# Performance work log

Measured on AMD Instinct MI355X. Metric: run time of the kernel, lower is better.

## Reference

```python
import jax, jax.numpy as jnp
import numpy as np

NUM_HEADS = 16


def setup_inputs() -> dict:
    key = jax.random.key(0)
    k1, k2, k3 = jax.random.split(key, 3)
    B, S, C = 1, 4096, 1024
    x = jax.random.normal(k1, (B, S, C), dtype=jnp.float32)
    # additive causal mask: 0 on/below diagonal, -1e9 above
    causal = jnp.triu(jnp.full((S, S), -1e9, dtype=jnp.float32), k=1)
    attention_mask = causal[None, None, :, :]
    W_attn = jax.random.normal(k2, (C, 3 * C), dtype=jnp.float32) * (C ** -0.5)
    b_attn = jnp.zeros((3 * C,), dtype=jnp.float32)
    W_proj = jax.random.normal(k3, (C, C), dtype=jnp.float32) * (C ** -0.5)
    b_proj = jnp.zeros((C,), dtype=jnp.float32)
    return {"x": x, "attention_mask": attention_mask, "W_attn": W_attn,
            "b_attn": b_attn, "W_proj": W_proj, "b_proj": b_proj}


def reference(x, attention_mask, W_attn, b_attn, W_proj, b_proj):
    B, S, C = x.shape
    H = NUM_HEADS
    hd = C // H
    qkv = x @ W_attn + b_attn                      # [B,S,3C]
    q, k, v = jnp.split(qkv, 3, axis=-1)
    # [B,S,C] -> [B,H,S,hd]
    q = q.reshape(B, S, H, hd).transpose(0, 2, 1, 3)
    k = k.reshape(B, S, H, hd).transpose(0, 2, 1, 3)
    v = v.reshape(B, S, H, hd).transpose(0, 2, 1, 3)
    att = jnp.einsum('bhqd,bhkd->bhqk', q, k) / jnp.sqrt(jnp.float32(hd))
    att = att + attention_mask                     # additive causal mask
    att = jax.nn.softmax(att, axis=-1)             # dropout is identity (p=0/eval)
    out = jnp.einsum('bhqk,bhkd->bhqd', att, v)    # [B,H,S,hd]
    out = out.transpose(0, 2, 1, 3).reshape(B, S, C)
    return out @ W_proj + b_proj
```

## Files before the change

kernel.cpp:

```cpp
#include <hip/hip_runtime.h>
#include <stdint.h>


typedef __bf16 bf16x8 __attribute__((ext_vector_type(8)));
typedef float f32x4 __attribute__((ext_vector_type(4)));

#define QSCALE 0.18033688011112042f

__device__ __forceinline__ f32x4 mfma16(bf16x8 a, bf16x8 b, f32x4 c) {
  return __builtin_amdgcn_mfma_f32_16x16x32_bf16(a, b, c, 0, 0, 0);
}

__device__ __forceinline__ void g2l16(const void* g, void* l) {
  __builtin_amdgcn_global_load_lds(
      (const __attribute__((address_space(1))) unsigned int*)g,
      (__attribute__((address_space(3))) unsigned int*)l,
      16, 0, 0);
}

__device__ __forceinline__ uint16_t f2bf(float f) {
  unsigned int u = __builtin_bit_cast(unsigned int, f);
  u += 0x7fffu + ((u >> 16) & 1u);
  return (uint16_t)(u >> 16);
}

__device__ __forceinline__ unsigned int pack_hi(float lo, float hi) {
  return __builtin_amdgcn_perm(__builtin_bit_cast(unsigned int, hi),
                               __builtin_bit_cast(unsigned int, lo), 0x07060302u);
}

__global__ __launch_bounds__(256) void f2b_k(const float* __restrict__ in,
                                             uint16_t* __restrict__ out, int n) {
  const int base = (blockIdx.x * 256 + threadIdx.x) * 8;
  if (base >= n) return;
  float4 a = *(const float4*)(in + base);
  float4 b = *(const float4*)(in + base + 4);
  uint16_t t[8];
  t[0] = f2bf(a.x); t[1] = f2bf(a.y); t[2] = f2bf(a.z); t[3] = f2bf(a.w);
  t[4] = f2bf(b.x); t[5] = f2bf(b.y); t[6] = f2bf(b.z); t[7] = f2bf(b.w);
  *(int4*)(out + base) = *(const int4*)t;
}

__global__ __launch_bounds__(256) void transpose2_f2b(const float* __restrict__ inA,
                                                      uint16_t* __restrict__ outA,
                                                      const float* __restrict__ inB,
                                                      uint16_t* __restrict__ outB) {
  __shared__ float t[64][65];
  const int tx = threadIdx.x & 15;
  const int ty = threadIdx.x >> 4;
  const bool isA = blockIdx.x < 48;
  const float* in = isA ? inA : inB;
  uint16_t* out = isA ? outA : outB;
  const int C = isA ? 3072 : 1024;
  const int bx = isA ? blockIdx.x : (blockIdx.x - 48);
  const int r0 = blockIdx.y * 64, c0 = bx * 64;
#pragma unroll
  for (int rr = ty; rr < 64; rr += 16) {
    float4 v = *(const float4*)(in + (size_t)(r0 + rr) * C + c0 + tx * 4);
    t[rr][tx * 4 + 0] = v.x; t[rr][tx * 4 + 1] = v.y;
    t[rr][tx * 4 + 2] = v.z; t[rr][tx * 4 + 3] = v.w;
  }
  __syncthreads();
#pragma unroll
  for (int cc = ty; cc < 64; cc += 16) {
    uint16_t tmp[4];
#pragma unroll
    for (int j = 0; j < 4; j++) tmp[j] = f2bf(t[tx * 4 + j][cc]);
    *(uint2*)(out + (size_t)(c0 + cc) * 1024 + r0 + tx * 4) = *(const uint2*)tmp;
  }
}

template <int EPI>
__global__ __launch_bounds__(256) void gemm_bt(const uint16_t* __restrict__ A,
                                               const uint16_t* __restrict__ Bt,
                                               const float* __restrict__ bias,
                                               uint16_t* __restrict__ outQ,
                                               uint16_t* __restrict__ outK,
                                               uint16_t* __restrict__ outV,
                                               float* __restrict__ outF) {
  __shared__ __align__(16) uint16_t lA[128 * 32];
  __shared__ __align__(16) uint16_t lB[128 * 32];
  const int tid = threadIdx.x;
  const int w = tid >> 6, lane = tid & 63;
  const int quad = lane >> 4, c16 = lane & 15;
  const int m0 = blockIdx.y * 128, n0 = blockIdx.x * 128;

  f32x4 acc[4][4];
#pragma unroll
  for (int i = 0; i < 4; i++)
#pragma unroll
    for (int j = 0; j < 4; j++) acc[i][j] = f32x4{0.f, 0.f, 0.f, 0.f};

  for (int k0 = 0; k0 < 1024; k0 += 32) {
    __syncthreads();
#pragma unroll
    for (int ii = 0; ii < 2; ii++) {
      const int instr = w * 2 + ii;
      const int p16 = instr * 64 + lane;
      const int row = p16 >> 2, cp = p16 & 3;
      const int c = cp ^ ((row >> 1) & 3);
      g2l16(A + (size_t)(m0 + row) * 1024 + k0 + c * 8, (char*)lA + (size_t)instr * 1024);
      g2l16(Bt + (size_t)(n0 + row) * 1024 + k0 + c * 8, (char*)lB + (size_t)instr * 1024);
    }
    __syncthreads();
    bf16x8 af[4], bfr[4];
#pragma unroll
    for (int t = 0; t < 4; t++) {
      const int mr = (w >> 1) * 64 + t * 16 + c16;
      af[t] = *(const bf16x8*)((const char*)lA + mr * 64 + ((quad ^ ((mr >> 1) & 3)) * 16));
      const int nr = (w & 1) * 64 + t * 16 + c16;
      bfr[t] = *(const bf16x8*)((const char*)lB + nr * 64 + ((quad ^ ((nr >> 1) & 3)) * 16));
    }
#pragma unroll
    for (int i = 0; i < 4; i++)
#pragma unroll
      for (int j = 0; j < 4; j++) acc[i][j] = mfma16(af[i], bfr[j], acc[i][j]);
  }

  const int mbase = m0 + (w >> 1) * 64;
  const int nbase = n0 + (w & 1) * 64;
  float bv[4];
#pragma unroll
  for (int j = 0; j < 4; j++) bv[j] = bias[nbase + j * 16 + c16];
#pragma unroll
  for (int i = 0; i < 4; i++) {
#pragma unroll
    for (int j = 0; j < 4; j++) {
      const int n = nbase + j * 16 + c16;
#pragma unroll
      for (int r = 0; r < 4; r++) {
        const int m = mbase + i * 16 + quad * 4 + r;
        float fv = acc[i][j][r] + bv[j];
        if (EPI == 0) {
          const int region = n >> 10;
          const int cr = n & 1023;
          const int h = cr >> 6, d = cr & 63;
          if (region == 0)      outQ[((size_t)(h << 12) + m) * 64 + d] = f2bf(fv * QSCALE);
          else if (region == 1) outK[((size_t)(h << 12) + m) * 64 + d] = f2bf(fv);
          else                  outV[(((size_t)(h * 32 + (m >> 7)) * 64 + d) << 7) + (m & 127)] = f2bf(fv);
        } else {
          outF[(size_t)m * 1024 + n] = fv;
        }
      }
    }
  }
}

__global__ __launch_bounds__(256, 2) void attn_kernel(const uint16_t* __restrict__ Qb,
                                                      const uint16_t* __restrict__ Kb,
                                                      const uint16_t* __restrict__ Vtb,
                                                      uint16_t* __restrict__ Ob) {
  __shared__ __align__(16) uint16_t lX[4][2][64 * 64];
  __shared__ float lL[4][64];
  const int tid = threadIdx.x;
  const int w = tid >> 6;
  const int lane = tid & 63;
  const int quad = lane >> 4, c16 = lane & 15;
  const int c7 = c16 & 7;
  const int bid = blockIdx.x;
  const int h = bid & 15;
  const int sw = 63 - (bid >> 4);
  const int q0w = sw * 64;
  const int jmax = sw >> 1;

  const int stage_off = (lane >> 3) * 64 + (((lane & 7) ^ (lane >> 3)) << 3);

#define STAGE_K(BUF, KBH)                                                       \
  _Pragma("unroll") for (int s = 0; s < 8; s++)                                 \
      g2l16((KBH) + s * 512 + stage_off, (char*)lX[w][BUF] + s * 1024);

  bf16x8 qf[4][2];
#pragma unroll
  for (int ntq = 0; ntq < 4; ntq++)
#pragma unroll
    for (int kc = 0; kc < 2; kc++) {
      int4 v = *(const int4*)(Qb + ((size_t)(h << 12) + q0w + ntq * 16 + c16) * 64 + kc * 32 + quad * 8);
      qf[ntq][kc] = __builtin_bit_cast(bf16x8, v);
    }

  float ls[4] = {0.f, 0.f, 0.f, 0.f};
  f32x4 o[4][4];
#pragma unroll
  for (int i = 0; i < 4; i++)
#pragma unroll
    for (int nq = 0; nq < 4; nq++) o[i][nq] = f32x4{0.f, 0.f, 0.f, 0.f};

  {
    const uint16_t* kb0 = Kb + ((size_t)(h << 12) + w * 128) * 64;
    STAGE_K(0, kb0);
  }

  for (int j = w; j <= jmax; j += 4) {
    const uint16_t* kbase = Kb + ((size_t)(h << 12) + j * 128) * 64;
    const uint16_t* vbase = Vtb + (((size_t)(h * 32 + j) * 64) << 7);

#pragma unroll
    for (int half = 0; half < 2; half++) {
      if (half == 0) {
        STAGE_K(1, kbase + 4096);
        asm volatile("s_waitcnt vmcnt(8)" ::: "memory");
      } else if (j + 4 <= jmax) {
        const uint16_t* kbn = Kb + ((size_t)(h << 12) + (j + 4) * 128) * 64;
        STAGE_K(0, kbn);
        asm volatile("s_waitcnt vmcnt(8)" ::: "memory");
      } else {
        asm volatile("s_waitcnt vmcnt(0)" ::: "memory");
      }

      bf16x8 kfr[2][4];
      const char* kx = (const char*)lX[w][half] + c16 * 128;
#pragma unroll
      for (int kc = 0; kc < 2; kc++)
#pragma unroll
        for (int mt = 0; mt < 4; mt++)
          kfr[kc][mt] = *(const bf16x8*)(kx + mt * 2048 + (((kc * 4 + quad) ^ c7) << 4));

#pragma unroll
      for (int qp = 0; qp < 2; qp++) {
        f32x4 st[4][2];
#pragma unroll
        for (int mt = 0; mt < 4; mt++) {
          st[mt][0] = f32x4{0.f, 0.f, 0.f, 0.f};
          st[mt][1] = f32x4{0.f, 0.f, 0.f, 0.f};
        }
        __builtin_amdgcn_s_setprio(1);
#pragma unroll
        for (int kc = 0; kc < 2; kc++)
#pragma unroll
          for (int mt = 0; mt < 4; mt++) {
            st[mt][0] = mfma16(kfr[kc][mt], qf[qp * 2 + 0][kc], st[mt][0]);
            st[mt][1] = mfma16(kfr[kc][mt], qf[qp * 2 + 1][kc], st[mt][1]);
          }
        __builtin_amdgcn_s_setprio(0);

        if (j == jmax) {
#pragma unroll
          for (int nt = 0; nt < 2; nt++) {
            const int qg = q0w + qp * 32 + nt * 16 + c16;
#pragma unroll
            for (int mt = 0; mt < 4; mt++)
#pragma unroll
              for (int rr = 0; rr < 4; rr++) {
                const int key = j * 128 + half * 64 + mt * 16 + quad * 4 + rr;
                if (key > qg) st[mt][nt][rr] = -1.0e9f;
              }
          }
        }

#pragma unroll
        for (int nt = 0; nt < 2; nt++) {
          float sum0 = 0.f, sum1 = 0.f;
          const int prow = qp * 32 + nt * 16 + c16;
          const size_t pbase = (size_t)prow * 128;
#pragma unroll
          for (int mt = 0; mt < 4; mt++) {
            float p0 = __builtin_amdgcn_exp2f(st[mt][nt][0]);
            float p1 = __builtin_amdgcn_exp2f(st[mt][nt][1]);
            float p2 = __builtin_amdgcn_exp2f(st[mt][nt][2]);
            float p3 = __builtin_amdgcn_exp2f(st[mt][nt][3]);
            sum0 += p0 + p1;
            sum1 += p2 + p3;
            const unsigned int lo = pack_hi(p0, p1);
            const unsigned int hi = pack_hi(p2, p3);
            const int chunk = mt * 2 + (quad >> 1);
            uint2* dst = (uint2*)((char*)lX[w][half] + pbase +
                                  ((chunk ^ (prow & 7)) << 4) + (quad & 1) * 8);
            *dst = make_uint2(lo, hi);
          }
          float sum = sum0 + sum1;
          sum += __shfl_xor(sum, 16);
          sum += __shfl_xor(sum, 32);
          ls[qp * 2 + nt] += sum;
        }
      }

#pragma unroll
      for (int kc2 = 0; kc2 < 2; kc2++) {
        int4 vf[4];
#pragma unroll
        for (int mt = 0; mt < 4; mt++)
          vf[mt] = *(const int4*)(vbase + ((mt * 16 + c16) << 7) +
                                  (half * 8 + kc2 * 4 + quad) * 8);
        bf16x8 pb[4];
#pragma unroll
        for (int ntq = 0; ntq < 4; ntq++) {
          const int prow = ntq * 16 + c16;
          pb[ntq] = *(const bf16x8*)((const char*)lX[w][half] + (size_t)prow * 128 +
                                     (((kc2 * 4 + quad) ^ (prow & 7)) << 4));
        }
        __builtin_amdgcn_s_setprio(1);
#pragma unroll
        for (int mt = 0; mt < 4; mt++) {
          bf16x8 a = __builtin_bit_cast(bf16x8, vf[mt]);
#pragma unroll
          for (int ntq = 0; ntq < 4; ntq++)
            o[mt][ntq] = mfma16(a, pb[ntq], o[mt][ntq]);
        }
        __builtin_amdgcn_s_setprio(0);
      }
    }
  }

  asm volatile("s_waitcnt vmcnt(0)" ::: "memory");

  float* oL = (float*)lX[w];
#pragma unroll
  for (int mt = 0; mt < 4; mt++)
#pragma unroll
    for (int ntq = 0; ntq < 4; ntq++)
#pragma unroll
      for (int rr = 0; rr < 4; rr++)
        oL[(mt * 16 + quad * 4 + rr) * 64 + ntq * 16 + c16] = o[mt][ntq][rr];
  if (quad == 0) {
#pragma unroll
    for (int ntq = 0; ntq < 4; ntq++) lL[w][ntq * 16 + c16] = ls[ntq];
  }
  __syncthreads();

  const int q = tid & 63, dq = tid >> 6;
  const float lsum = lL[0][q] + lL[1][q] + lL[2][q] + lL[3][q];
  const float inv = 1.f / lsum;
  uint16_t t[16] __attribute__((aligned(16)));
#pragma unroll
  for (int i = 0; i < 16; i++) {
    const int d = dq * 16 + i;
    const int off = d * 64 + q;
    float s = ((const float*)lX[0])[off] + ((const float*)lX[1])[off] +
              ((const float*)lX[2])[off] + ((const float*)lX[3])[off];
    t[i] = f2bf(s * inv);
  }
  uint16_t* dst = Ob + (size_t)(q0w + q) * 1024 + h * 64 + dq * 16;
  *(int4*)dst = *(const int4*)t;
  *(int4*)(dst + 8) = *(const int4*)(t + 8);
#undef STAGE_K
}

extern "C" void kernel_launch(void* const* d_in, const int* in_sizes, int n_in,
                              void* d_out, int out_size, void* d_ws, size_t ws_size,
                              hipStream_t stream) {
  const float* x      = (const float*)d_in[0];
  const float* W_attn = (const float*)d_in[2];
  const float* b_attn = (const float*)d_in[3];
  const float* W_proj = (const float*)d_in[4];
  const float* b_proj = (const float*)d_in[5];
  float* out = (float*)d_out;

  char* ws = (char*)d_ws;
  uint16_t* Ob  = (uint16_t*)(ws);
  uint16_t* wtA = (uint16_t*)(ws + 8388608);
  uint16_t* wtP = (uint16_t*)(ws + 14680064);
  uint16_t* Qb  = (uint16_t*)(ws + 16777216);
  uint16_t* Kb  = (uint16_t*)(ws + 25165824);
  uint16_t* Vtb = (uint16_t*)(ws + 33554432);
  uint16_t* xb  = (uint16_t*)(ws + 41943040);

  f2b_k<<<2048, 256, 0, stream>>>(x, xb, 4096 * 1024);
  transpose2_f2b<<<dim3(64, 16), 256, 0, stream>>>(W_attn, wtA, W_proj, wtP);
  gemm_bt<0><<<dim3(24, 32), 256, 0, stream>>>(xb, wtA, b_attn, Qb, Kb, Vtb, nullptr);
  attn_kernel<<<dim3(1024), 256, 0, stream>>>(Qb, Kb, Vtb, Ob);
  gemm_bt<1><<<dim3(8, 32), 256, 0, stream>>>(Ob, wtP, b_proj, nullptr, nullptr, nullptr, out);
}
```

Measured before the change: 239.8 us.

## Double-buffer GEMM LDS tiles and swizzle workgroup order across XCDs

The projection GEMM now uses two LDS buffers for the A and B tiles. It issues the global-to-LDS load for the next K slice before running the MFMAs on the current one, which cuts one barrier per iteration and overlaps load latency with math. Workgroup IDs are also remapped so that consecutive blocks sent to the same XCD cover neighbouring output tiles, which should improve L2 reuse. LDS use doubles, and the remap assumes the grid size is a multiple of 8.

After: 238.4 us. Within noise of the previous version (-0.6%).

```diff
diff --git a/kernel.cpp b/kernel.cpp
--- a/kernel.cpp
+++ b/kernel.cpp
@@ -78,12 +78,16 @@
                                                uint16_t* __restrict__ outK,
                                                uint16_t* __restrict__ outV,
                                                float* __restrict__ outF) {
-  __shared__ __align__(16) uint16_t lA[128 * 32];
-  __shared__ __align__(16) uint16_t lB[128 * 32];
+  __shared__ __align__(16) uint16_t lA[2][128 * 32];
+  __shared__ __align__(16) uint16_t lB[2][128 * 32];
   const int tid = threadIdx.x;
   const int w = tid >> 6, lane = tid & 63;
   const int quad = lane >> 4, c16 = lane & 15;
-  const int m0 = blockIdx.y * 128, n0 = blockIdx.x * 128;
+
+  const int nwg = gridDim.x * gridDim.y;
+  const int lin = blockIdx.y * gridDim.x + blockIdx.x;
+  const int swz = (lin & 7) * (nwg >> 3) + (lin >> 3);
+  const int m0 = (swz / gridDim.x) * 128, n0 = (swz % gridDim.x) * 128;
 
   f32x4 acc[4][4];
 #pragma unroll
@@ -91,30 +95,41 @@
 #pragma unroll
     for (int j = 0; j < 4; j++) acc[i][j] = f32x4{0.f, 0.f, 0.f, 0.f};
 
+  const int instr = w * 2;
+#define STAGE(BUF, K0)                                                          \
+  _Pragma("unroll") for (int ii = 0; ii < 2; ii++) {                            \
+    const int p16 = (instr + ii) * 64 + lane;                                   \
+    const int row = p16 >> 2, cp = p16 & 3;                                     \
+    const int c = cp ^ ((row >> 1) & 3);                                        \
+    g2l16(A + (size_t)(m0 + row) * 1024 + (K0) + c * 8,                         \
+          (char*)lA[BUF] + (size_t)(instr + ii) * 1024);                        \
+    g2l16(Bt + (size_t)(n0 + row) * 1024 + (K0) + c * 8,                        \
+          (char*)lB[BUF] + (size_t)(instr + ii) * 1024);                        \
+  }
+
+  STAGE(0, 0);
+  asm volatile("s_waitcnt vmcnt(0)" ::: "memory");
+  __syncthreads();
+
+  int cur = 0;
   for (int k0 = 0; k0 < 1024; k0 += 32) {
-    __syncthreads();
-#pragma unroll
-    for (int ii = 0; ii < 2; ii++) {
-      const int instr = w * 2 + ii;
-      const int p16 = instr * 64 + lane;
-      const int row = p16 >> 2, cp = p16 & 3;
-      const int c = cp ^ ((row >> 1) & 3);
-      g2l16(A + (size_t)(m0 + row) * 1024 + k0 + c * 8, (char*)lA + (size_t)instr * 1024);
-      g2l16(Bt + (size_t)(n0 + row) * 1024 + k0 + c * 8, (char*)lB + (size_t)instr * 1024);
-    }
-    __syncthreads();
+    if (k0 + 32 < 1024) STAGE(cur ^ 1, k0 + 32);
+
     bf16x8 af[4], bfr[4];
 #pragma unroll
     for (int t = 0; t < 4; t++) {
       const int mr = (w >> 1) * 64 + t * 16 + c16;
-      af[t] = *(const bf16x8*)((const char*)lA + mr * 64 + ((quad ^ ((mr >> 1) & 3)) * 16));
+      af[t] = *(const bf16x8*)((const char*)lA[cur] + mr * 64 + ((quad ^ ((mr >> 1) & 3)) * 16));
       const int nr = (w & 1) * 64 + t * 16 + c16;
-      bfr[t] = *(const bf16x8*)((const char*)lB + nr * 64 + ((quad ^ ((nr >> 1) & 3)) * 16));
+      bfr[t] = *(const bf16x8*)((const char*)lB[cur] + nr * 64 + ((quad ^ ((nr >> 1) & 3)) * 16));
     }
 #pragma unroll
     for (int i = 0; i < 4; i++)
 #pragma unroll
       for (int j = 0; j < 4; j++) acc[i][j] = mfma16(af[i], bfr[j], acc[i][j]);
+
+    __syncthreads();
+    cur ^= 1;
   }
 
   const int mbase = m0 + (w >> 1) * 64;
@@ -144,6 +159,7 @@
       }
     }
   }
+#undef STAGE
 }
 
 __global__ __launch_bounds__(256, 2) void attn_kernel(const uint16_t* __restrict__ Qb,
```
